# Kernel tuning notes

Hardware: AMD Instinct MI355X
Metric: run time of the kernel (lower is better)

The kernel has to match this reference:

```python
import jax, jax.numpy as jnp
from jax import lax
import numpy as np

B, L, M, D, K, STRIDE = 32, 32768, 32, 128, 16, 8


def setup_inputs() -> dict:
    key = jax.random.key(0)
    k1, k2, k3, k4 = jax.random.split(key, 4)
    x = jax.random.normal(k1, (B, L, M), dtype=jnp.float32)
    # sorted timestamps per sample, like torch.sort(rand*100)
    timestamps = jnp.sort(jax.random.uniform(k2, (B, L), dtype=jnp.float32) * 100.0, axis=1)
    fan_in = M * K
    bound = 1.0 / np.sqrt(fan_in)
    conv_w = jax.random.uniform(k3, (D, M, K), dtype=jnp.float32, minval=-bound, maxval=bound)
    conv_b = jax.random.uniform(k4, (D,), dtype=jnp.float32, minval=-bound, maxval=bound)
    return {"x": x, "timestamps": timestamps, "conv_w": conv_w, "conv_b": conv_b}


def reference(x, timestamps, conv_w, conv_b):
    # Conv1d patch embedding: x [B,L,M] -> NCL -> conv -> [B,P,D]
    patches = lax.conv_general_dilated(
        x.transpose(0, 2, 1), conv_w,
        window_strides=(STRIDE,), padding=[(0, 0)],
        dimension_numbers=("NCH", "OIH", "NCH"))
    patches = patches.transpose(0, 2, 1) + conv_b  # [B,P,D]
    P = patches.shape[1]

    # Per-patch median timestamp (padding=0 -> all windows full length K).
    # torch.median on even-length returns the LOWER median = sorted idx (K-1)//2.
    starts = jnp.arange(P) * STRIDE
    idx = starts[:, None] + jnp.arange(K)          # [P,K]
    windows = timestamps[:, idx]                   # [B,P,K]
    med = jnp.sort(windows, axis=-1)[..., (K - 1) // 2]  # [B,P]

    # Sinusoidal PE at continuous times.
    div_term = jnp.exp(jnp.arange(0, D, 2).astype(jnp.float32) * (-np.log(10000.0) / D))
    ang = med[..., None] * div_term                # [B,P,D//2]
    pe = jnp.stack([jnp.sin(ang), jnp.cos(ang)], axis=-1).reshape(med.shape[0], P, D)
    return patches + pe
```

## Files before the change

kernel.cpp:

```cpp
#include <hip/hip_runtime.h>
#include <hip/hip_bf16.h>

#define Bn 32
#define Ln 32768
#define Mn 32
#define Dn 128
#define Pn 4095
#define KKn 512

typedef short  bf16x8 __attribute__((ext_vector_type(8)));
typedef float  f32x4  __attribute__((ext_vector_type(4)));

union BU { bf16x8 v; unsigned short u[8]; };

static __device__ __forceinline__ unsigned short f2bf(float f) {
  __hip_bfloat16 h = __float2bfloat16(f);
  return *reinterpret_cast<unsigned short*>(&h);
}

__global__ __launch_bounds__(256) void prep_w_kernel(const float* __restrict__ w,
                                                     unsigned short* __restrict__ wswz) {
  int idx = blockIdx.x * 256 + threadIdx.x;
  int j = idx & 7;
  int d = (idx >> 3) & 127;
  int g = idx >> 10;
  int kk = g * 8 + j;
  int k = kk >> 5;
  int m = kk & 31;
  wswz[idx] = f2bf(w[(d << 9) + (m << 4) + k]);
}

__global__ __launch_bounds__(256, 4) void gemm_pe_kernel(
    const float* __restrict__ x,
    const float* __restrict__ ts,
    const unsigned short* __restrict__ wswz,
    const float* __restrict__ bias,
    float* __restrict__ out) {

  __shared__ unsigned short xs[2080 * 8];

  const int b   = blockIdx.y;
  const int pt0 = blockIdx.x;
  const int tid = threadIdx.x;

  const float* xsrc = x + (size_t)b * Ln * Mn + (size_t)pt0 * 512 * Mn;
  const int r0 = pt0 * 512;
  for (int g = tid; g < 2080; g += 256) {
    int s = g * 8;
    int row = r0 + (s >> 5);
    float4 f0, f1;
    if (row < Ln) {
      f0 = *reinterpret_cast<const float4*>(xsrc + s);
      f1 = *reinterpret_cast<const float4*>(xsrc + s + 4);
    } else {
      f0 = make_float4(0.f, 0.f, 0.f, 0.f);
      f1 = f0;
    }
    BU bu;
    bu.u[0] = f2bf(f0.x); bu.u[1] = f2bf(f0.y); bu.u[2] = f2bf(f0.z); bu.u[3] = f2bf(f0.w);
    bu.u[4] = f2bf(f1.x); bu.u[5] = f2bf(f1.y); bu.u[6] = f2bf(f1.z); bu.u[7] = f2bf(f1.w);
    int phys = (g & ~7) | ((g & 7) ^ ((g >> 5) & 7));
    *reinterpret_cast<bf16x8*>(&xs[phys * 8]) = bu.v;
  }
  __syncthreads();

  const int lane = tid & 63;
  const int wv   = tid >> 6;
  const int mrow = lane & 15;
  const int quad = lane >> 4;

  f32x4 acc[4][2] = {};

  #pragma unroll
  for (int t = 0; t < 16; ++t) {
    bf16x8 afrag[4];
    #pragma unroll
    for (int pt = 0; pt < 4; ++pt) {
      int p_loc = pt * 16 + mrow;
      int g = p_loc * 32 + t * 4 + quad;
      int phys = (g & ~7) | ((g & 7) ^ ((g >> 5) & 7));
      afrag[pt] = *reinterpret_cast<const bf16x8*>(&xs[phys * 8]);
    }
    bf16x8 bfrag[2];
    #pragma unroll
    for (int dt = 0; dt < 2; ++dt) {
      int d = wv * 32 + dt * 16 + mrow;
      bfrag[dt] = *reinterpret_cast<const bf16x8*>(
          &wswz[((((t << 2) + quad) << 7) + d) << 3]);
    }
    #pragma unroll
    for (int pt = 0; pt < 4; ++pt)
      #pragma unroll
      for (int dt = 0; dt < 2; ++dt)
        acc[pt][dt] = __builtin_amdgcn_mfma_f32_16x16x32_bf16(
            afrag[pt], bfrag[dt], acc[pt][dt], 0, 0, 0);
  }

  const float NEG_C = -0.14391156831212810f;
  float div[2], phs;
  {
    int d0 = wv * 32 + mrow;
    div[0] = __expf(NEG_C * (float)(d0 >> 1));
    div[1] = __expf(NEG_C * (float)((d0 + 16) >> 1));
    phs = (d0 & 1) ? 1.5707963267948966f : 0.0f;
  }
  const float* tsb = ts + (size_t)b * Ln;
  #pragma unroll
  for (int pt = 0; pt < 4; ++pt) {
    #pragma unroll
    for (int reg = 0; reg < 4; ++reg) {
      int p = pt0 * 64 + pt * 16 + quad * 4 + reg;
      if (p < Pn) {
        float med = tsb[p * 8 + 7];
        size_t ob = ((size_t)b * Pn + p) * Dn;
        #pragma unroll
        for (int dt = 0; dt < 2; ++dt) {
          int d = wv * 32 + dt * 16 + mrow;
          float pe = sinf(med * div[dt] + phs);
          out[ob + d] = acc[pt][dt][reg] + bias[d] + pe;
        }
      }
    }
  }
}

extern "C" void kernel_launch(void* const* d_in, const int* in_sizes, int n_in,
                              void* d_out, int out_size, void* d_ws, size_t ws_size,
                              hipStream_t stream) {
  const float* x      = (const float*)d_in[0];
  const float* ts     = (const float*)d_in[1];
  const float* conv_w = (const float*)d_in[2];
  const float* conv_b = (const float*)d_in[3];
  float* out = (float*)d_out;
  unsigned short* wswz = (unsigned short*)d_ws;

  prep_w_kernel<<<256, 256, 0, stream>>>(conv_w, wswz);
  gemm_pe_kernel<<<dim3(64, Bn), 256, 0, stream>>>(x, ts, wswz, conv_b, out);
}
```

Baseline: 248.6 us.

## Batch x loads, prefetch MFMA fragments, stage medians in LDS, use fast sin

Issues all eight per-thread float4 pairs of x before converting any of them, so more global loads are in flight at once. Software-pipelines the GEMM loop by prefetching the next A fragments from LDS and keeping B fragments three steps ahead in a rotating register buffer. Median timestamps are staged once in shared memory and read as a vector, and bias and the PE frequencies are hoisted out of the epilogue. The epilogue swaps the precise sinf for __sinf, which is cheaper but less accurate for arguments up to about 100, and the deeper prefetching raises register pressure.

```diff
diff --git a/kernel.cpp b/kernel.cpp
--- a/kernel.cpp
+++ b/kernel.cpp
@@ -16,6 +16,10 @@
 static __device__ __forceinline__ unsigned short f2bf(float f) {
   __hip_bfloat16 h = __float2bfloat16(f);
   return *reinterpret_cast<unsigned short*>(&h);
+}
+
+static __device__ __forceinline__ int swz(int g) {
+  return (g & ~7) | ((g & 7) ^ ((g >> 5) & 7));
 }
 
 __global__ __launch_bounds__(256) void prep_w_kernel(const float* __restrict__ w,
@@ -38,87 +42,122 @@
     float* __restrict__ out) {
 
   __shared__ unsigned short xs[2080 * 8];
+  __shared__ float tsl[64];
 
   const int b   = blockIdx.y;
   const int pt0 = blockIdx.x;
   const int tid = threadIdx.x;
-
-  const float* xsrc = x + (size_t)b * Ln * Mn + (size_t)pt0 * 512 * Mn;
-  const int r0 = pt0 * 512;
-  for (int g = tid; g < 2080; g += 256) {
-    int s = g * 8;
-    int row = r0 + (s >> 5);
-    float4 f0, f1;
-    if (row < Ln) {
-      f0 = *reinterpret_cast<const float4*>(xsrc + s);
-      f1 = *reinterpret_cast<const float4*>(xsrc + s + 4);
-    } else {
-      f0 = make_float4(0.f, 0.f, 0.f, 0.f);
-      f1 = f0;
-    }
-    BU bu;
-    bu.u[0] = f2bf(f0.x); bu.u[1] = f2bf(f0.y); bu.u[2] = f2bf(f0.z); bu.u[3] = f2bf(f0.w);
-    bu.u[4] = f2bf(f1.x); bu.u[5] = f2bf(f1.y); bu.u[6] = f2bf(f1.z); bu.u[7] = f2bf(f1.w);
-    int phys = (g & ~7) | ((g & 7) ^ ((g >> 5) & 7));
-    *reinterpret_cast<bf16x8*>(&xs[phys * 8]) = bu.v;
-  }
-  __syncthreads();
-
   const int lane = tid & 63;
   const int wv   = tid >> 6;
   const int mrow = lane & 15;
   const int quad = lane >> 4;
 
+  const int d0 = wv * 32 + mrow;
+  const float NEG_C = -0.14391156831212810f;
+  const float div0 = __expf(NEG_C * (float)(d0 >> 1));
+  const float div1 = __expf(NEG_C * (float)((d0 + 16) >> 1));
+  const float phs  = (d0 & 1) ? 1.5707963267948966f : 0.0f;
+  const float bias0 = bias[d0];
+  const float bias1 = bias[d0 + 16];
+
+  const float* xsrc = x + (size_t)b * Ln * Mn + (size_t)pt0 * 512 * Mn;
+  const int r0 = pt0 * 512;
+
+  float4 f[8][2];
+  #pragma unroll
+  for (int i = 0; i < 8; ++i) {
+    int g = i * 256 + tid;
+    const float4* src = reinterpret_cast<const float4*>(xsrc) + (size_t)g * 2;
+    f[i][0] = src[0];
+    f[i][1] = src[1];
+  }
+  if (tid >= 64 && tid < 128) {
+    int pl = tid - 64;
+    tsl[pl] = ts[(size_t)b * Ln + r0 + pl * 8 + 7];
+  }
+  #pragma unroll
+  for (int i = 0; i < 8; ++i) {
+    int g = i * 256 + tid;
+    BU bu;
+    bu.u[0] = f2bf(f[i][0].x); bu.u[1] = f2bf(f[i][0].y);
+    bu.u[2] = f2bf(f[i][0].z); bu.u[3] = f2bf(f[i][0].w);
+    bu.u[4] = f2bf(f[i][1].x); bu.u[5] = f2bf(f[i][1].y);
+    bu.u[6] = f2bf(f[i][1].z); bu.u[7] = f2bf(f[i][1].w);
+    *reinterpret_cast<bf16x8*>(&xs[swz(g) * 8]) = bu.v;
+  }
+  if (tid < 32) {
+    int g = 2048 + tid;
+    BU bu;
+    if (pt0 < 63) {
+      const float4* src = reinterpret_cast<const float4*>(xsrc) + (size_t)g * 2;
+      float4 t0 = src[0], t1 = src[1];
+      bu.u[0] = f2bf(t0.x); bu.u[1] = f2bf(t0.y); bu.u[2] = f2bf(t0.z); bu.u[3] = f2bf(t0.w);
+      bu.u[4] = f2bf(t1.x); bu.u[5] = f2bf(t1.y); bu.u[6] = f2bf(t1.z); bu.u[7] = f2bf(t1.w);
+    } else {
+      bu.v = (bf16x8)0;
+    }
+    *reinterpret_cast<bf16x8*>(&xs[swz(g) * 8]) = bu.v;
+  }
+  __syncthreads();
+
+  int agbase[4];
+  #pragma unroll
+  for (int pt = 0; pt < 4; ++pt) agbase[pt] = (pt * 16 + mrow) * 32 + quad;
+  const unsigned short* bbase = wswz + (((quad << 7) + (wv << 5) + mrow) << 3);
+
   f32x4 acc[4][2] = {};
+
+  bf16x8 a_cur[4];
+  #pragma unroll
+  for (int pt = 0; pt < 4; ++pt)
+    a_cur[pt] = *reinterpret_cast<const bf16x8*>(&xs[swz(agbase[pt]) * 8]);
+
+  bf16x8 bp[3][2];
+  #pragma unroll
+  for (int j = 0; j < 3; ++j) {
+    bp[j][0] = *reinterpret_cast<const bf16x8*>(bbase + j * 4096);
+    bp[j][1] = *reinterpret_cast<const bf16x8*>(bbase + 128 + j * 4096);
+  }
 
   #pragma unroll
   for (int t = 0; t < 16; ++t) {
-    bf16x8 afrag[4];
+    const int cur = t % 3;
+    bf16x8 a_nxt[4];
+    if (t < 15) {
+      #pragma unroll
+      for (int pt = 0; pt < 4; ++pt)
+        a_nxt[pt] = *reinterpret_cast<const bf16x8*>(&xs[swz(agbase[pt] + (t + 1) * 4) * 8]);
+    }
+    bf16x8 bc0 = bp[cur][0], bc1 = bp[cur][1];
+    if (t < 13) {
+      bp[cur][0] = *reinterpret_cast<const bf16x8*>(bbase + (t + 3) * 4096);
+      bp[cur][1] = *reinterpret_cast<const bf16x8*>(bbase + 128 + (t + 3) * 4096);
+    }
     #pragma unroll
     for (int pt = 0; pt < 4; ++pt) {
-      int p_loc = pt * 16 + mrow;
-      int g = p_loc * 32 + t * 4 + quad;
-      int phys = (g & ~7) | ((g & 7) ^ ((g >> 5) & 7));
-      afrag[pt] = *reinterpret_cast<const bf16x8*>(&xs[phys * 8]);
+      acc[pt][0] = __builtin_amdgcn_mfma_f32_16x16x32_bf16(a_cur[pt], bc0, acc[pt][0], 0, 0, 0);
+      acc[pt][1] = __builtin_amdgcn_mfma_f32_16x16x32_bf16(a_cur[pt], bc1, acc[pt][1], 0, 0, 0);
     }
-    bf16x8 bfrag[2];
-    #pragma unroll
-    for (int dt = 0; dt < 2; ++dt) {
-      int d = wv * 32 + dt * 16 + mrow;
-      bfrag[dt] = *reinterpret_cast<const bf16x8*>(
-          &wswz[((((t << 2) + quad) << 7) + d) << 3]);
+    if (t < 15) {
+      #pragma unroll
+      for (int pt = 0; pt < 4; ++pt) a_cur[pt] = a_nxt[pt];
     }
-    #pragma unroll
-    for (int pt = 0; pt < 4; ++pt)
-      #pragma unroll
-      for (int dt = 0; dt < 2; ++dt)
-        acc[pt][dt] = __builtin_amdgcn_mfma_f32_16x16x32_bf16(
-            afrag[pt], bfrag[dt], acc[pt][dt], 0, 0, 0);
   }
 
-  const float NEG_C = -0.14391156831212810f;
-  float div[2], phs;
-  {
-    int d0 = wv * 32 + mrow;
-    div[0] = __expf(NEG_C * (float)(d0 >> 1));
-    div[1] = __expf(NEG_C * (float)((d0 + 16) >> 1));
-    phs = (d0 & 1) ? 1.5707963267948966f : 0.0f;
-  }
-  const float* tsb = ts + (size_t)b * Ln;
   #pragma unroll
   for (int pt = 0; pt < 4; ++pt) {
+    const int plbase = pt * 16 + quad * 4;
+    f32x4 med4 = *reinterpret_cast<const f32x4*>(&tsl[plbase]);
+    const int pbase = pt0 * 64 + plbase;
+    float* obase = out + ((size_t)b * Pn + pbase) * Dn + d0;
     #pragma unroll
     for (int reg = 0; reg < 4; ++reg) {
-      int p = pt0 * 64 + pt * 16 + quad * 4 + reg;
-      if (p < Pn) {
-        float med = tsb[p * 8 + 7];
-        size_t ob = ((size_t)b * Pn + p) * Dn;
-        #pragma unroll
-        for (int dt = 0; dt < 2; ++dt) {
-          int d = wv * 32 + dt * 16 + mrow;
-          float pe = sinf(med * div[dt] + phs);
-          out[ob + d] = acc[pt][dt][reg] + bias[d] + pe;
-        }
+      if (pbase + reg < Pn) {
+        float m = med4[reg];
+        float pe0 = __sinf(m * div0 + phs);
+        float pe1 = __sinf(m * div1 + phs);
+        obase[reg * Dn]      = acc[pt][0][reg] + bias0 + pe0;
+        obase[reg * Dn + 16] = acc[pt][1][reg] + bias1 + pe1;
       }
     }
   }
```

Result: faster. 225.8 us (-9.2%).

## Load conv inputs straight into registers with double-buffered prefetch, drop LDS staging

Applied to the files above, without the earlier changes.

The shared-memory staging of x is removed. Each wave now loads its overlapping conv windows directly from global memory as fp32, converts them to bf16 in registers and prefetches the next k-step while the current MFMAs run. The bf16 weight fragments are double-buffered the same way. Waves are rearranged into a 2x2 tile of 32 patches by 64 channels, with launch bounds lowered to 3 blocks per CU. The epilogue hoists bias loads and the median-timestamp loads, and swaps sinf for the faster, less accurate __sinf. The aim is to remove the LDS round trip and barrier and to cut transcendental cost. In exchange, overlapping windows are re-read from global memory and cache, register pressure rises, and accuracy of sine at arguments near 100 drops.

```diff
diff --git a/kernel.cpp b/kernel.cpp
--- a/kernel.cpp
+++ b/kernel.cpp
@@ -18,6 +18,13 @@
   return *reinterpret_cast<unsigned short*>(&h);
 }
 
+static __device__ __forceinline__ bf16x8 cvt8(const float4& a, const float4& b) {
+  BU bu;
+  bu.u[0] = f2bf(a.x); bu.u[1] = f2bf(a.y); bu.u[2] = f2bf(a.z); bu.u[3] = f2bf(a.w);
+  bu.u[4] = f2bf(b.x); bu.u[5] = f2bf(b.y); bu.u[6] = f2bf(b.z); bu.u[7] = f2bf(b.w);
+  return bu.v;
+}
+
 __global__ __launch_bounds__(256) void prep_w_kernel(const float* __restrict__ w,
                                                      unsigned short* __restrict__ wswz) {
   int idx = blockIdx.x * 256 + threadIdx.x;
@@ -30,94 +37,106 @@
   wswz[idx] = f2bf(w[(d << 9) + (m << 4) + k]);
 }
 
-__global__ __launch_bounds__(256, 4) void gemm_pe_kernel(
+__global__ __launch_bounds__(256, 3) void gemm_pe_kernel(
     const float* __restrict__ x,
     const float* __restrict__ ts,
     const unsigned short* __restrict__ wswz,
     const float* __restrict__ bias,
     float* __restrict__ out) {
 
-  __shared__ unsigned short xs[2080 * 8];
-
   const int b   = blockIdx.y;
   const int pt0 = blockIdx.x;
   const int tid = threadIdx.x;
-
-  const float* xsrc = x + (size_t)b * Ln * Mn + (size_t)pt0 * 512 * Mn;
-  const int r0 = pt0 * 512;
-  for (int g = tid; g < 2080; g += 256) {
-    int s = g * 8;
-    int row = r0 + (s >> 5);
-    float4 f0, f1;
-    if (row < Ln) {
-      f0 = *reinterpret_cast<const float4*>(xsrc + s);
-      f1 = *reinterpret_cast<const float4*>(xsrc + s + 4);
-    } else {
-      f0 = make_float4(0.f, 0.f, 0.f, 0.f);
-      f1 = f0;
-    }
-    BU bu;
-    bu.u[0] = f2bf(f0.x); bu.u[1] = f2bf(f0.y); bu.u[2] = f2bf(f0.z); bu.u[3] = f2bf(f0.w);
-    bu.u[4] = f2bf(f1.x); bu.u[5] = f2bf(f1.y); bu.u[6] = f2bf(f1.z); bu.u[7] = f2bf(f1.w);
-    int phys = (g & ~7) | ((g & 7) ^ ((g >> 5) & 7));
-    *reinterpret_cast<bf16x8*>(&xs[phys * 8]) = bu.v;
-  }
-  __syncthreads();
-
   const int lane = tid & 63;
   const int wv   = tid >> 6;
   const int mrow = lane & 15;
   const int quad = lane >> 4;
+  const int wp = wv & 1;
+  const int wd = wv >> 1;
 
-  f32x4 acc[4][2] = {};
+  const float* xb = x + (size_t)b * (Ln * Mn);
+  const float* ap[2];
+  #pragma unroll
+  for (int pt = 0; pt < 2; ++pt) {
+    int p = pt0 * 64 + wp * 32 + pt * 16 + mrow;
+    int pc = (p < Pn) ? p : 0;
+    ap[pt] = xb + (size_t)pc * 256 + quad * 8;
+  }
+  const unsigned short* bq = wswz + (((quad << 7) + (wd << 6) + mrow) << 3);
+
+  float4 ar[2][2][2];
+  #pragma unroll
+  for (int pt = 0; pt < 2; ++pt) {
+    ar[0][pt][0] = *reinterpret_cast<const float4*>(ap[pt]);
+    ar[0][pt][1] = *reinterpret_cast<const float4*>(ap[pt] + 4);
+  }
+  bf16x8 bp[2][4];
+  #pragma unroll
+  for (int dt = 0; dt < 4; ++dt)
+    bp[0][dt] = *reinterpret_cast<const bf16x8*>(bq + dt * 128);
+  #pragma unroll
+  for (int dt = 0; dt < 4; ++dt)
+    bp[1][dt] = *reinterpret_cast<const bf16x8*>(bq + 4096 + dt * 128);
+  bq += 8192;
+
+  f32x4 acc[2][4] = {};
 
   #pragma unroll
   for (int t = 0; t < 16; ++t) {
-    bf16x8 afrag[4];
+    const int cur = t & 1, nxt = cur ^ 1;
+    if (t < 15) {
+      #pragma unroll
+      for (int pt = 0; pt < 2; ++pt) {
+        ar[nxt][pt][0] = *reinterpret_cast<const float4*>(ap[pt] + (t + 1) * 32);
+        ar[nxt][pt][1] = *reinterpret_cast<const float4*>(ap[pt] + (t + 1) * 32 + 4);
+      }
+    }
+    bf16x8 bc[4];
     #pragma unroll
-    for (int pt = 0; pt < 4; ++pt) {
-      int p_loc = pt * 16 + mrow;
-      int g = p_loc * 32 + t * 4 + quad;
-      int phys = (g & ~7) | ((g & 7) ^ ((g >> 5) & 7));
-      afrag[pt] = *reinterpret_cast<const bf16x8*>(&xs[phys * 8]);
+    for (int dt = 0; dt < 4; ++dt) bc[dt] = bp[cur][dt];
+    if (t < 14) {
+      #pragma unroll
+      for (int dt = 0; dt < 4; ++dt)
+        bp[cur][dt] = *reinterpret_cast<const bf16x8*>(bq + dt * 128);
+      bq += 4096;
     }
-    bf16x8 bfrag[2];
+    bf16x8 af[2];
     #pragma unroll
-    for (int dt = 0; dt < 2; ++dt) {
-      int d = wv * 32 + dt * 16 + mrow;
-      bfrag[dt] = *reinterpret_cast<const bf16x8*>(
-          &wswz[((((t << 2) + quad) << 7) + d) << 3]);
-    }
+    for (int pt = 0; pt < 2; ++pt) af[pt] = cvt8(ar[cur][pt][0], ar[cur][pt][1]);
     #pragma unroll
-    for (int pt = 0; pt < 4; ++pt)
+    for (int pt = 0; pt < 2; ++pt)
       #pragma unroll
-      for (int dt = 0; dt < 2; ++dt)
+      for (int dt = 0; dt < 4; ++dt)
         acc[pt][dt] = __builtin_amdgcn_mfma_f32_16x16x32_bf16(
-            afrag[pt], bfrag[dt], acc[pt][dt], 0, 0, 0);
+            af[pt], bc[dt], acc[pt][dt], 0, 0, 0);
   }
 
+  const int d0 = wd * 64 + mrow;
   const float NEG_C = -0.14391156831212810f;
-  float div[2], phs;
-  {
-    int d0 = wv * 32 + mrow;
-    div[0] = __expf(NEG_C * (float)(d0 >> 1));
-    div[1] = __expf(NEG_C * (float)((d0 + 16) >> 1));
-    phs = (d0 & 1) ? 1.5707963267948966f : 0.0f;
+  float div4[4], bias4[4];
+  #pragma unroll
+  for (int dt = 0; dt < 4; ++dt) {
+    div4[dt]  = __expf(NEG_C * (float)((d0 + dt * 16) >> 1));
+    bias4[dt] = bias[d0 + dt * 16];
   }
+  const float phs = (d0 & 1) ? 1.5707963267948966f : 0.0f;
   const float* tsb = ts + (size_t)b * Ln;
+
   #pragma unroll
-  for (int pt = 0; pt < 4; ++pt) {
+  for (int pt = 0; pt < 2; ++pt) {
+    const int pbase = pt0 * 64 + wp * 32 + pt * 16 + quad * 4;
+    float* ob = out + ((size_t)b * Pn + pbase) * Dn + d0;
+    float med[4];
+    #pragma unroll
+    for (int reg = 0; reg < 4; ++reg)
+      med[reg] = tsb[(pbase + reg) * 8 + 7];
     #pragma unroll
     for (int reg = 0; reg < 4; ++reg) {
-      int p = pt0 * 64 + pt * 16 + quad * 4 + reg;
-      if (p < Pn) {
-        float med = tsb[p * 8 + 7];
-        size_t ob = ((size_t)b * Pn + p) * Dn;
+      if (pbase + reg < Pn) {
         #pragma unroll
-        for (int dt = 0; dt < 2; ++dt) {
-          int d = wv * 32 + dt * 16 + mrow;
-          float pe = sinf(med * div[dt] + phs);
-          out[ob + d] = acc[pt][dt][reg] + bias[d] + pe;
+        for (int dt = 0; dt < 4; ++dt) {
+          float pe = __sinf(med[reg] * div4[dt] + phs);
+          ob[reg * Dn + dt * 16] = acc[pt][dt][reg] + bias4[dt] + pe;
         }
       }
     }
```

After: 279.2 us. +12.3%, slower.

## Stage x tiles via direct global-to-LDS loads and halve tile per block

Applied to the files above, without the earlier changes.

Replaces the register-staged fp32-to-bf16 conversion of the x tile with asynchronous global_load_lds copies of raw fp32 into swizzled shared memory. The bf16 conversion now happens when fragments are read for the MFMAs. Each block now covers 32 patches instead of 64, so the grid doubles. Weight fragments are prefetched through a three-deep register ring, and medians are staged in LDS. The epilogue switches sinf to the faster, less accurate __sinf and hoists the bias loads. The changes target load latency and occupancy, but they double LDS traffic per element and add conversion work inside the MFMA loop.

```diff
diff --git a/kernel.cpp b/kernel.cpp
--- a/kernel.cpp
+++ b/kernel.cpp
@@ -10,12 +10,25 @@
 
 typedef short  bf16x8 __attribute__((ext_vector_type(8)));
 typedef float  f32x4  __attribute__((ext_vector_type(4)));
+typedef __attribute__((address_space(3))) unsigned int       lds_u32;
+typedef const __attribute__((address_space(1))) unsigned int glb_u32;
 
 union BU { bf16x8 v; unsigned short u[8]; };
 
 static __device__ __forceinline__ unsigned short f2bf(float f) {
   __hip_bfloat16 h = __float2bfloat16(f);
   return *reinterpret_cast<unsigned short*>(&h);
+}
+
+static __device__ __forceinline__ bf16x8 cvt8(const f32x4& a, const f32x4& b) {
+  BU bu;
+  bu.u[0] = f2bf(a[0]); bu.u[1] = f2bf(a[1]); bu.u[2] = f2bf(a[2]); bu.u[3] = f2bf(a[3]);
+  bu.u[4] = f2bf(b[0]); bu.u[5] = f2bf(b[1]); bu.u[6] = f2bf(b[2]); bu.u[7] = f2bf(b[3]);
+  return bu.v;
+}
+
+static __device__ __forceinline__ int phi(int g) {
+  return g ^ ((g >> 6) & 7);
 }
 
 __global__ __launch_bounds__(256) void prep_w_kernel(const float* __restrict__ w,
@@ -37,88 +50,97 @@
     const float* __restrict__ bias,
     float* __restrict__ out) {
 
-  __shared__ unsigned short xs[2080 * 8];
+  __shared__ float xsf[9216];
+  __shared__ float tsl[32];
 
-  const int b   = blockIdx.y;
-  const int pt0 = blockIdx.x;
-  const int tid = threadIdx.x;
-
-  const float* xsrc = x + (size_t)b * Ln * Mn + (size_t)pt0 * 512 * Mn;
-  const int r0 = pt0 * 512;
-  for (int g = tid; g < 2080; g += 256) {
-    int s = g * 8;
-    int row = r0 + (s >> 5);
-    float4 f0, f1;
-    if (row < Ln) {
-      f0 = *reinterpret_cast<const float4*>(xsrc + s);
-      f1 = *reinterpret_cast<const float4*>(xsrc + s + 4);
-    } else {
-      f0 = make_float4(0.f, 0.f, 0.f, 0.f);
-      f1 = f0;
-    }
-    BU bu;
-    bu.u[0] = f2bf(f0.x); bu.u[1] = f2bf(f0.y); bu.u[2] = f2bf(f0.z); bu.u[3] = f2bf(f0.w);
-    bu.u[4] = f2bf(f1.x); bu.u[5] = f2bf(f1.y); bu.u[6] = f2bf(f1.z); bu.u[7] = f2bf(f1.w);
-    int phys = (g & ~7) | ((g & 7) ^ ((g >> 5) & 7));
-    *reinterpret_cast<bf16x8*>(&xs[phys * 8]) = bu.v;
-  }
-  __syncthreads();
-
+  const int b    = blockIdx.y;
+  const int tile = blockIdx.x;
+  const int tid  = threadIdx.x;
   const int lane = tid & 63;
   const int wv   = tid >> 6;
   const int mrow = lane & 15;
   const int quad = lane >> 4;
 
-  f32x4 acc[4][2] = {};
+  if (tid < 32)
+    tsl[tid] = ts[(size_t)b * Ln + tile * 256 + tid * 8 + 7];
+
+  {
+    const size_t slab0g = (((size_t)b * Ln * Mn) >> 2) + (size_t)tile * 2048;
+    const size_t xg_max = (((size_t)Bn * Ln * Mn) >> 2) - 1;
+    #pragma unroll
+    for (int j = 0; j < 9; ++j) {
+      const int Pw = wv * 576 + j * 64;
+      const int P  = Pw + lane;
+      size_t gg = slab0g + (size_t)phi(P);
+      if (gg > xg_max) gg = xg_max;
+      __builtin_amdgcn_global_load_lds((glb_u32*)(x + (gg << 2)),
+                                       (lds_u32*)&xsf[(size_t)Pw << 2], 16, 0, 0);
+    }
+  }
+
+  const unsigned short* bq = wswz + (((quad << 7) + (wv << 5) + mrow) << 3);
+  bf16x8 bp[3][2];
+  #pragma unroll
+  for (int j = 0; j < 3; ++j) {
+    bp[j][0] = *reinterpret_cast<const bf16x8*>(bq + j * 4096);
+    bp[j][1] = *reinterpret_cast<const bf16x8*>(bq + j * 4096 + 128);
+  }
+
+  __syncthreads();
+
+  int agbase[2];
+  #pragma unroll
+  for (int pt = 0; pt < 2; ++pt) agbase[pt] = (pt * 16 + mrow) * 64 + quad * 2;
+
+  f32x4 acc[2][2] = {};
 
   #pragma unroll
   for (int t = 0; t < 16; ++t) {
-    bf16x8 afrag[4];
+    const int cur = t % 3;
+    bf16x8 af[2];
     #pragma unroll
-    for (int pt = 0; pt < 4; ++pt) {
-      int p_loc = pt * 16 + mrow;
-      int g = p_loc * 32 + t * 4 + quad;
-      int phys = (g & ~7) | ((g & 7) ^ ((g >> 5) & 7));
-      afrag[pt] = *reinterpret_cast<const bf16x8*>(&xs[phys * 8]);
+    for (int pt = 0; pt < 2; ++pt) {
+      const int G  = agbase[pt] + t * 8;
+      const int gl = phi(G);
+      const int gh = gl ^ 1;
+      f32x4 lo = *reinterpret_cast<const f32x4*>(&xsf[gl * 4]);
+      f32x4 hi = *reinterpret_cast<const f32x4*>(&xsf[gh * 4]);
+      af[pt] = cvt8(lo, hi);
     }
-    bf16x8 bfrag[2];
-    #pragma unroll
-    for (int dt = 0; dt < 2; ++dt) {
-      int d = wv * 32 + dt * 16 + mrow;
-      bfrag[dt] = *reinterpret_cast<const bf16x8*>(
-          &wswz[((((t << 2) + quad) << 7) + d) << 3]);
+    bf16x8 bc0 = bp[cur][0], bc1 = bp[cur][1];
+    if (t < 13) {
+      bp[cur][0] = *reinterpret_cast<const bf16x8*>(bq + (t + 3) * 4096);
+      bp[cur][1] = *reinterpret_cast<const bf16x8*>(bq + (t + 3) * 4096 + 128);
     }
     #pragma unroll
-    for (int pt = 0; pt < 4; ++pt)
-      #pragma unroll
-      for (int dt = 0; dt < 2; ++dt)
-        acc[pt][dt] = __builtin_amdgcn_mfma_f32_16x16x32_bf16(
-            afrag[pt], bfrag[dt], acc[pt][dt], 0, 0, 0);
+    for (int pt = 0; pt < 2; ++pt) {
+      acc[pt][0] = __builtin_amdgcn_mfma_f32_16x16x32_bf16(af[pt], bc0, acc[pt][0], 0, 0, 0);
+      acc[pt][1] = __builtin_amdgcn_mfma_f32_16x16x32_bf16(af[pt], bc1, acc[pt][1], 0, 0, 0);
+    }
   }
 
+  const int d0 = wv * 32 + mrow;
   const float NEG_C = -0.14391156831212810f;
-  float div[2], phs;
-  {
-    int d0 = wv * 32 + mrow;
-    div[0] = __expf(NEG_C * (float)(d0 >> 1));
-    div[1] = __expf(NEG_C * (float)((d0 + 16) >> 1));
-    phs = (d0 & 1) ? 1.5707963267948966f : 0.0f;
-  }
-  const float* tsb = ts + (size_t)b * Ln;
+  const float div0  = __expf(NEG_C * (float)(d0 >> 1));
+  const float div1  = __expf(NEG_C * (float)((d0 + 16) >> 1));
+  const float phs   = (d0 & 1) ? 1.5707963267948966f : 0.0f;
+  const float bias0 = bias[d0];
+  const float bias1 = bias[d0 + 16];
+
   #pragma unroll
-  for (int pt = 0; pt < 4; ++pt) {
+  for (int pt = 0; pt < 2; ++pt) {
+    const int plbase = pt * 16 + quad * 4;
+    f32x4 med4 = *reinterpret_cast<const f32x4*>(&tsl[plbase]);
+    const int pbase = tile * 32 + plbase;
+    float* ob = out + ((size_t)b * Pn + pbase) * Dn + d0;
     #pragma unroll
     for (int reg = 0; reg < 4; ++reg) {
-      int p = pt0 * 64 + pt * 16 + quad * 4 + reg;
-      if (p < Pn) {
-        float med = tsb[p * 8 + 7];
-        size_t ob = ((size_t)b * Pn + p) * Dn;
-        #pragma unroll
-        for (int dt = 0; dt < 2; ++dt) {
-          int d = wv * 32 + dt * 16 + mrow;
-          float pe = sinf(med * div[dt] + phs);
-          out[ob + d] = acc[pt][dt][reg] + bias[d] + pe;
-        }
+      if (pbase + reg < Pn) {
+        float m = med4[reg];
+        float pe0 = __sinf(m * div0 + phs);
+        float pe1 = __sinf(m * div1 + phs);
+        ob[reg * Dn]      = acc[pt][0][reg] + bias0 + pe0;
+        ob[reg * Dn + 16] = acc[pt][1][reg] + bias1 + pe1;
       }
     }
   }
@@ -135,5 +157,5 @@
   unsigned short* wswz = (unsigned short*)d_ws;
 
   prep_w_kernel<<<256, 256, 0, stream>>>(conv_w, wswz);
-  gemm_pe_kernel<<<dim3(64, Bn), 256, 0, stream>>>(x, ts, wswz, conv_b, out);
+  gemm_pe_kernel<<<dim3(128, Bn), 256, 0, stream>>>(x, ts, wswz, conv_b, out);
 }
```

Result: faster. 229.2 us (-7.8%).
